# Performance work log

Measured on AMD Instinct MI355X. Metric: run time of the kernel, lower is better.

## Reference

```python
import jax, jax.numpy as jnp
import numpy as np

N = 100000      # nodes
E = 1600000     # edges
D = 128         # embedding_size (num_heads=1)
L = 4           # num_layers
NEG_SLOPE_ATT = 0.2    # GATConv attention LeakyReLU
NEG_SLOPE_ACT = 0.01   # nn.LeakyReLU default
LN_EPS = 1e-5


def leaky(x, s):
    return jnp.where(x > 0, x, s * x)


def layer_norm(x, gamma, beta):
    mu = jnp.mean(x, axis=-1, keepdims=True)
    var = jnp.mean(jnp.square(x - mu), axis=-1, keepdims=True)
    return (x - mu) * jax.lax.rsqrt(var + LN_EPS) * gamma + beta


def gat_conv(x, src, dst, W, a_src, a_dst, b):
    # PyG GATConv, heads=1, add_self_loops=False, no edge features
    h = x @ W                                  # [N, D]
    alpha_src = h @ a_src                      # [N]
    alpha_dst = h @ a_dst                      # [N]
    e = leaky(alpha_src[src] + alpha_dst[dst], NEG_SLOPE_ATT)   # [E]
    # softmax over incoming edges of each destination node
    m = jax.ops.segment_max(e, dst, num_segments=N)             # [N]
    ex = jnp.exp(e - m[dst])
    denom = jax.ops.segment_sum(ex, dst, num_segments=N)        # [N]
    alpha = ex / (denom[dst] + 1e-16)                           # [E]
    out = jax.ops.segment_sum(alpha[:, None] * h[src], dst, num_segments=N)
    return out + b


def setup_inputs() -> dict:
    key = jax.random.key(0)
    ks = jax.random.split(key, 12)
    x = jax.random.normal(ks[0], (N, D), dtype=jnp.float32)
    edge_index = jax.random.randint(ks[1], (2, E), 0, N, dtype=jnp.int32)
    s = 0.05
    return {
        "x": x,
        "edge_index": edge_index,
        "W_in": jax.random.normal(ks[2], (D, D), dtype=jnp.float32) * s,
        "b_in": jnp.zeros((D,), dtype=jnp.float32),
        "Wl": jax.random.normal(ks[3], (L, D, D), dtype=jnp.float32) * s,
        "att_src": jax.random.normal(ks[4], (L, D), dtype=jnp.float32) * s,
        "att_dst": jax.random.normal(ks[5], (L, D), dtype=jnp.float32) * s,
        "bias_l": jnp.zeros((L, D), dtype=jnp.float32),
        "gamma": jnp.ones((L, D), dtype=jnp.float32),
        "beta": jnp.zeros((L, D), dtype=jnp.float32),
    }


def reference(x, edge_index, W_in, b_in, Wl, att_src, att_dst, bias_l, gamma, beta):
    src, dst = edge_index[0], edge_index[1]
    h = leaky(x @ W_in + b_in, NEG_SLOPE_ACT)
    for i in range(L):
        h = gat_conv(h, src, dst, Wl[i], att_src[i], att_dst[i], bias_l[i])
        h = layer_norm(h, gamma[i], beta[i])
        h = leaky(h, NEG_SLOPE_ACT)
        # dropout p=0.3 is identity in eval mode; pooling undefined in source -> identity
    return h
```

## Files before the change

### kernel.cpp

```cpp
#include <hip/hip_runtime.h>
#include <hip/hip_fp16.h>
#include <math.h>

#define NN 100000
#define EE 1600000
#define DD 128
#define NBUCK 196
#define NBLKP 196
#define EPB 8192

typedef _Float16 f16;
typedef f16 f16x8 __attribute__((ext_vector_type(8)));
typedef float f32x4 __attribute__((ext_vector_type(4)));

#define LDA 136
#define WCHUNKS 2304

__global__ __launch_bounds__(256) void part_hist_k(const int* __restrict__ dst, int* __restrict__ bcnt) {
    __shared__ int lc[NBUCK];
    int t = threadIdx.x, blk = blockIdx.x;
    if (t < NBUCK) lc[t] = 0;
    __syncthreads();
    int e0 = blk * EPB;
    for (int i = t; i < EPB; i += 256) {
        int e = e0 + i;
        if (e < EE) atomicAdd(&lc[dst[e] >> 9], 1);
    }
    __syncthreads();
    if (t < NBUCK) bcnt[t * NBLKP + blk] = lc[t];
}

__global__ __launch_bounds__(256) void scanBB_k(const int* __restrict__ bcnt, int* __restrict__ ebase,
                                                int* __restrict__ btot) {
    __shared__ int sh[256];
    int t = threadIdx.x, b = blockIdx.x;
    int c = (t < NBLKP) ? bcnt[b * NBLKP + t] : 0;
    sh[t] = c;
    __syncthreads();
    for (int off = 1; off < 256; off <<= 1) {
        int v = (t >= off) ? sh[t - off] : 0;
        __syncthreads();
        sh[t] += v;
        __syncthreads();
    }
    if (t < NBLKP) ebase[b * NBLKP + t] = sh[t] - c;
    if (t == 255) btot[b] = sh[255];
}

__global__ __launch_bounds__(256) void scanBT_k(const int* __restrict__ btot, int* __restrict__ bstart,
                                                int* __restrict__ offsets) {
    __shared__ int sh[256];
    int t = threadIdx.x;
    int c = (t < NBUCK) ? btot[t] : 0;
    sh[t] = c;
    __syncthreads();
    for (int off = 1; off < 256; off <<= 1) {
        int v = (t >= off) ? sh[t - off] : 0;
        __syncthreads();
        sh[t] += v;
        __syncthreads();
    }
    if (t < NBUCK) bstart[t] = sh[t] - c;
    if (t == 0) { bstart[NBUCK] = EE; offsets[NN] = EE; }
}

__global__ __launch_bounds__(256) void part_k(const int* __restrict__ src, const int* __restrict__ dst,
                                              const int* __restrict__ bstart, const int* __restrict__ ebase,
                                              int2* __restrict__ ebuf) {
    __shared__ int cur[NBUCK];
    int t = threadIdx.x, blk = blockIdx.x;
    if (t < NBUCK) cur[t] = bstart[t] + ebase[t * NBLKP + blk];
    __syncthreads();
    int e0 = blk * EPB;
    for (int i = t; i < EPB; i += 256) {
        int e = e0 + i;
        if (e < EE) {
            int s = src[e], d = dst[e];
            int p = atomicAdd(&cur[d >> 9], 1);
            ebuf[p] = make_int2(s, d);
        }
    }
}

__global__ __launch_bounds__(512) void bucket_sort_k(const int2* __restrict__ ebuf,
                                                     const int* __restrict__ bstart,
                                                     int* __restrict__ offsets,
                                                     int* __restrict__ ssrc,
                                                     int* __restrict__ sdst) {
    __shared__ int sh[512];
    __shared__ int cur[512];
    int t = threadIdx.x, b = blockIdx.x;
    int d0 = b << 9;
    int beg = bstart[b], end = bstart[b + 1];

    cur[t] = 0;
    __syncthreads();
    for (int e = beg + t; e < end; e += 512) atomicAdd(&cur[ebuf[e].y - d0], 1);
    __syncthreads();
    int c = cur[t];
    sh[t] = c;
    __syncthreads();
    for (int off = 1; off < 512; off <<= 1) {
        int v = (t >= off) ? sh[t - off] : 0;
        __syncthreads();
        sh[t] += v;
        __syncthreads();
    }
    int excl = sh[t] - c;
    if (d0 + t < NN) offsets[d0 + t] = beg + excl;
    cur[t] = beg + excl;
    __syncthreads();
    for (int e = beg + t; e < end; e += 512) {
        int2 ed = ebuf[e];
        int p = atomicAdd(&cur[ed.y - d0], 1);
        ssrc[p] = ed.x;
        sdst[p] = ed.y;
    }
}

__global__ __launch_bounds__(256) void wprep_k(const float* __restrict__ W_in,
                                               const float* __restrict__ Wl,
                                               f16* __restrict__ Wt) {
    int m = blockIdx.x;
    const float* src = (m == 0) ? W_in : (Wl + (size_t)(m - 1) * DD * DD);
    f16* dst = Wt + (size_t)m * (WCHUNKS * 8);
    for (int q = 0; q < 64; ++q) {
        int idx = q * 256 + threadIdx.x;
        int k = idx >> 7, n = idx & 127;
        dst[n * LDA + k] = (f16)src[idx];
    }
}

template <int MODE, int F32IN>
__global__ __launch_bounds__(256, 2) void gemm_k(const void* __restrict__ Xv,
                                                 const f16* __restrict__ Wt,
                                                 const float* __restrict__ bias,
                                                 const float* __restrict__ av_src,
                                                 const float* __restrict__ av_dst,
                                                 __half* __restrict__ Yh,
                                                 float* __restrict__ alpha_src,
                                                 float* __restrict__ alpha_dst) {
    __shared__ __align__(16) f16 sA[128 * LDA];
    __shared__ __align__(16) f16 sW[WCHUNKS * 8];
    int t = threadIdx.x;
    int w = t >> 6, lane = t & 63;
    int row0 = blockIdx.x * 128;

    {
        const uint4* wsrc = (const uint4*)Wt;
        uint4* wdst = (uint4*)sW;
#pragma unroll
        for (int it = 0; it < 9; ++it) wdst[it * 256 + t] = wsrc[it * 256 + t];
    }
    if (F32IN) {
        const float* X = (const float*)Xv;
#pragma unroll
        for (int q = 0; q < 8; ++q) {
            int id = q * 256 + t;
            int r = id >> 4, c = id & 15;
            int grow = row0 + r;
            float4 a = make_float4(0.f, 0.f, 0.f, 0.f), b = a;
            if (grow < NN) {
                const float4* p = (const float4*)(X + (size_t)grow * DD + c * 8);
                a = p[0]; b = p[1];
            }
            union { f16 h[8]; uint4 u; } H;
            H.h[0] = (f16)a.x; H.h[1] = (f16)a.y; H.h[2] = (f16)a.z; H.h[3] = (f16)a.w;
            H.h[4] = (f16)b.x; H.h[5] = (f16)b.y; H.h[6] = (f16)b.z; H.h[7] = (f16)b.w;
            *(uint4*)(sA + r * LDA + c * 8) = H.u;
        }
    } else {
        const __half* X = (const __half*)Xv;
#pragma unroll
        for (int q = 0; q < 8; ++q) {
            int id = q * 256 + t;
            int r = id >> 4, c = id & 15;
            int grow = row0 + r;
            uint4 v = make_uint4(0, 0, 0, 0);
            if (grow < NN) v = ((const uint4*)(X + (size_t)grow * DD))[c];
            *(uint4*)(sA + r * LDA + c * 8) = v;
        }
    }
    __syncthreads();

    int cl = lane & 15, qw = lane >> 4;
    f32x4 acc[2][8] = {};
#pragma unroll
    for (int ks = 0; ks < 4; ++ks) {
        int koff = ks * 32 + qw * 8;
        f16x8 bh[8];
#pragma unroll
        for (int nf = 0; nf < 8; ++nf)
            bh[nf] = *(const f16x8*)(sW + (nf * 16 + cl) * LDA + koff);
#pragma unroll
        for (int rf = 0; rf < 2; ++rf) {
            f16x8 ah = *(const f16x8*)(sA + (w * 32 + rf * 16 + cl) * LDA + koff);
#pragma unroll
            for (int nf = 0; nf < 8; ++nf)
                acc[rf][nf] = __builtin_amdgcn_mfma_f32_16x16x32_f16(ah, bh[nf], acc[rf][nf], 0, 0, 0);
        }
    }

    if (MODE == 0) {
        float bc[8];
#pragma unroll
        for (int nf = 0; nf < 8; ++nf) bc[nf] = bias[nf * 16 + cl];
#pragma unroll
        for (int rf = 0; rf < 2; ++rf) {
            int rbase = row0 + w * 32 + rf * 16 + qw * 4;
#pragma unroll
            for (int i = 0; i < 4; ++i) {
                int row = rbase + i;
                if (row < NN) {
#pragma unroll
                    for (int nf = 0; nf < 8; ++nf) {
                        float v = acc[rf][nf][i] + bc[nf];
                        v = v > 0.f ? v : 0.01f * v;
                        Yh[(size_t)row * DD + nf * 16 + cl] = __float2half(v);
                    }
                }
            }
        }
    } else {
        float as[8], ad[8];
#pragma unroll
        for (int nf = 0; nf < 8; ++nf) {
            as[nf] = av_src[nf * 16 + cl];
            ad[nf] = av_dst[nf * 16 + cl];
        }
#pragma unroll
        for (int rf = 0; rf < 2; ++rf) {
            int rbase = row0 + w * 32 + rf * 16 + qw * 4;
            float pa[4] = {0.f, 0.f, 0.f, 0.f}, pb[4] = {0.f, 0.f, 0.f, 0.f};
#pragma unroll
            for (int nf = 0; nf < 8; ++nf) {
#pragma unroll
                for (int i = 0; i < 4; ++i) {
                    float v = acc[rf][nf][i];
                    pa[i] += v * as[nf];
                    pb[i] += v * ad[nf];
                }
            }
#pragma unroll
            for (int i = 0; i < 4; ++i) {
                int row = rbase + i;
                if (row < NN) {
#pragma unroll
                    for (int nf = 0; nf < 8; ++nf)
                        Yh[(size_t)row * DD + nf * 16 + cl] = __float2half(acc[rf][nf][i]);
                }
            }
#pragma unroll
            for (int i = 0; i < 4; ++i) {
#pragma unroll
                for (int off = 8; off >= 1; off >>= 1) {
                    pa[i] += __shfl_xor(pa[i], off);
                    pb[i] += __shfl_xor(pb[i], off);
                }
            }
            if (cl == 0) {
#pragma unroll
                for (int i = 0; i < 4; ++i) {
                    int row = rbase + i;
                    if (row < NN) {
                        alpha_src[row] = pa[i];
                        alpha_dst[row] = pb[i];
                    }
                }
            }
        }
    }
}

__global__ __launch_bounds__(256) void edgew_k(const int* __restrict__ ssrc,
                                               const int* __restrict__ sdst,
                                               const float* __restrict__ alpha_src,
                                               const float* __restrict__ alpha_dst,
                                               int2* __restrict__ epk) {
    int j = blockIdx.x * 256 + threadIdx.x;
    if (j < EE) {
        int s = ssrc[j];
        float e = alpha_src[s] + alpha_dst[sdst[j]];
        e = e > 0.f ? e : 0.2f * e;
        epk[j] = make_int2(s, __float_as_int(__expf(e)));
    } else if (j < EE + 16) {
        epk[j] = make_int2(0, 0);
    }
}

template <int HOUT>
__global__ __launch_bounds__(256) void agg_k(const __half* __restrict__ tmp,
                                             const int2* __restrict__ epk,
                                             const int* __restrict__ offsets,
                                             const float* __restrict__ bias,
                                             const float* __restrict__ gamma,
                                             const float* __restrict__ beta,
                                             void* __restrict__ outv) {
    int wid = (blockIdx.x * 256 + threadIdx.x) >> 6;
    wid = __builtin_amdgcn_readfirstlane(wid);
    int lane = threadIdx.x & 63;
    int beg = __builtin_amdgcn_readfirstlane(offsets[wid]);
    int end = __builtin_amdgcn_readfirstlane(offsets[wid + 1]);

    const __half2* tmp2 = (const __half2*)tmp;
    float ax0 = 0.f, ay0 = 0.f, ax1 = 0.f, ay1 = 0.f, dsum = 0.f;

    for (int j = (beg & ~1); j < end; j += 16) {
        int4 q[8];
#pragma unroll
        for (int k = 0; k < 8; ++k) q[k] = *(const int4*)(epk + j + 2 * k);
        __half2 h[16];
#pragma unroll
        for (int k = 0; k < 8; ++k) {
            h[2 * k]     = tmp2[(size_t)q[k].x * 64 + lane];
            h[2 * k + 1] = tmp2[(size_t)q[k].z * 64 + lane];
        }
#pragma unroll
        for (int k = 0; k < 8; ++k) {
            int e0 = j + 2 * k, e1 = e0 + 1;
            bool v0 = (k == 0) ? (e0 >= beg && e0 < end) : (e0 < end);
            bool v1 = (e1 < end);
            float w0 = v0 ? __int_as_float(q[k].y) : 0.f;
            float w1 = v1 ? __int_as_float(q[k].w) : 0.f;
            dsum += w0 + w1;
            ax0 = fmaf(w0, __half2float(h[2 * k].x), ax0);
            ay0 = fmaf(w0, __half2float(h[2 * k].y), ay0);
            ax1 = fmaf(w1, __half2float(h[2 * k + 1].x), ax1);
            ay1 = fmaf(w1, __half2float(h[2 * k + 1].y), ay1);
        }
    }

    float inv = 1.0f / (dsum + 1e-16f);

    float ax = (ax0 + ax1) * inv + bias[2 * lane];
    float ay = (ay0 + ay1) * inv + bias[2 * lane + 1];

    float s1 = ax + ay;
#pragma unroll
    for (int off = 32; off >= 1; off >>= 1) s1 += __shfl_xor(s1, off);
    float mu = s1 * (1.0f / 128.0f);
    float dx = ax - mu, dy = ay - mu;
    float s2 = dx * dx + dy * dy;
#pragma unroll
    for (int off = 32; off >= 1; off >>= 1) s2 += __shfl_xor(s2, off);
    float rstd = rsqrtf(s2 * (1.0f / 128.0f) + 1e-5f);

    float yx = dx * rstd * gamma[2 * lane] + beta[2 * lane];
    float yy = dy * rstd * gamma[2 * lane + 1] + beta[2 * lane + 1];
    yx = yx > 0.f ? yx : 0.01f * yx;
    yy = yy > 0.f ? yy : 0.01f * yy;
    if (HOUT) {
        ((__half2*)outv)[(size_t)wid * 64 + lane] = __floats2half2_rn(yx, yy);
    } else {
        ((float2*)outv)[(size_t)wid * 64 + lane] = make_float2(yx, yy);
    }
}

extern "C" void kernel_launch(void* const* d_in, const int* in_sizes, int n_in,
                              void* d_out, int out_size, void* d_ws, size_t ws_size,
                              hipStream_t stream) {
    const float* x       = (const float*)d_in[0];
    const int*   ei      = (const int*)d_in[1];
    const float* W_in    = (const float*)d_in[2];
    const float* b_in    = (const float*)d_in[3];
    const float* Wl      = (const float*)d_in[4];
    const float* att_src = (const float*)d_in[5];
    const float* att_dst = (const float*)d_in[6];
    const float* bias_l  = (const float*)d_in[7];
    const float* gamma   = (const float*)d_in[8];
    const float* beta    = (const float*)d_in[9];
    float* out = (float*)d_out;

    char* ws = (char*)d_ws;
    __half* tmp      = (__half*)ws; ws += (size_t)NN * DD * 2;
    float* alpha_src = (float*)ws;  ws += (size_t)NN * 4;
    float* alpha_dst = (float*)ws;  ws += (size_t)NN * 4;
    int*   offsets   = (int*)ws;    ws += (size_t)(NN + 4) * 4;
    int*   ssrc      = (int*)ws;    ws += (size_t)EE * 4;
    int*   sdst      = (int*)ws;    ws += (size_t)EE * 4;
    int2*  ebuf      = (int2*)ws;   ws += (size_t)(EE + 16) * 8;
    int*   bcnt      = (int*)ws;    ws += (size_t)NBUCK * NBLKP * 4;
    int*   ebase     = (int*)ws;    ws += (size_t)NBUCK * NBLKP * 4;
    int*   btot      = (int*)ws;    ws += (size_t)(NBUCK + 4) * 4;
    int*   bstart    = (int*)ws;    ws += (size_t)(NBUCK + 4) * 4;
    f16*   Wt        = (f16*)ws;    ws += (size_t)5 * WCHUNKS * 16;
    int2* epk = ebuf;

    __half* hbuf = (__half*)d_out;

    const int* esrc = ei;
    const int* edst = ei + EE;

    part_hist_k<<<NBLKP, 256, 0, stream>>>(edst, bcnt);
    scanBB_k<<<NBUCK, 256, 0, stream>>>(bcnt, ebase, btot);
    scanBT_k<<<1, 256, 0, stream>>>(btot, bstart, offsets);
    part_k<<<NBLKP, 256, 0, stream>>>(esrc, edst, bstart, ebase, ebuf);
    bucket_sort_k<<<NBUCK, 512, 0, stream>>>(ebuf, bstart, offsets, ssrc, sdst);
    wprep_k<<<5, 256, 0, stream>>>(W_in, Wl, Wt);

    const int gg = (NN + 127) / 128;
    const int eg = (EE + 16 + 255) / 256;

    gemm_k<0, 1><<<gg, 256, 0, stream>>>(x, Wt, b_in, nullptr, nullptr, hbuf, nullptr, nullptr);

    for (int i = 0; i < 4; i++) {
        gemm_k<1, 0><<<gg, 256, 0, stream>>>(hbuf, Wt + (size_t)(i + 1) * (WCHUNKS * 8), nullptr,
                                             att_src + (size_t)i * DD, att_dst + (size_t)i * DD,
                                             tmp, alpha_src, alpha_dst);
        edgew_k<<<eg, 256, 0, stream>>>(ssrc, sdst, alpha_src, alpha_dst, epk);
        if (i < 3) {
            agg_k<1><<<NN / 4, 256, 0, stream>>>(tmp, epk, offsets,
                                                 bias_l + (size_t)i * DD, gamma + (size_t)i * DD,
                                                 beta + (size_t)i * DD, (void*)hbuf);
        } else {
            agg_k<0><<<NN / 4, 256, 0, stream>>>(tmp, epk, offsets,
                                                 bias_l + (size_t)i * DD, gamma + (size_t)i * DD,
                                                 beta + (size_t)i * DD, (void*)out);
        }
    }
}
```

Before: 580.4 us.

## Load GEMM A operands directly to registers and split aggregation lanes across edge pairs

The GEMM kernel no longer stages the activation tile in shared memory. Each wave loads its A fragments straight from global memory into registers, and the occupancy hint rises to 3 blocks per CU. The aggregation kernel now has each half-wave handle alternate edges with 8-byte gathers of 4 features per lane. Each 16-edge chunk is accumulated with packed half-precision FMAs, then the two halves are combined with a cross-half shuffle. This cuts LDS traffic and the number of gather instructions, at the cost of reduced accumulation precision from fp16 partial sums.

```diff
diff --git a/kernel.cpp b/kernel.cpp
--- a/kernel.cpp
+++ b/kernel.cpp
@@ -132,7 +132,7 @@
 }
 
 template <int MODE, int F32IN>
-__global__ __launch_bounds__(256, 2) void gemm_k(const void* __restrict__ Xv,
+__global__ __launch_bounds__(256, 3) void gemm_k(const void* __restrict__ Xv,
                                                  const f16* __restrict__ Wt,
                                                  const float* __restrict__ bias,
                                                  const float* __restrict__ av_src,
@@ -140,11 +140,42 @@
                                                  __half* __restrict__ Yh,
                                                  float* __restrict__ alpha_src,
                                                  float* __restrict__ alpha_dst) {
-    __shared__ __align__(16) f16 sA[128 * LDA];
     __shared__ __align__(16) f16 sW[WCHUNKS * 8];
     int t = threadIdx.x;
     int w = t >> 6, lane = t & 63;
+    int cl = lane & 15, qw = lane >> 4;
     int row0 = blockIdx.x * 128;
+
+    f16x8 a[2][4];
+    if (F32IN) {
+        const float* X = (const float*)Xv;
+#pragma unroll
+        for (int rf = 0; rf < 2; ++rf) {
+            int row = row0 + w * 32 + rf * 16 + cl;
+            row = row < NN ? row : NN - 1;
+            const float* p = X + (size_t)row * DD;
+#pragma unroll
+            for (int ks = 0; ks < 4; ++ks) {
+                float4 u0 = *(const float4*)(p + ks * 32 + qw * 8);
+                float4 u1 = *(const float4*)(p + ks * 32 + qw * 8 + 4);
+                f16x8 v;
+                v[0] = (f16)u0.x; v[1] = (f16)u0.y; v[2] = (f16)u0.z; v[3] = (f16)u0.w;
+                v[4] = (f16)u1.x; v[5] = (f16)u1.y; v[6] = (f16)u1.z; v[7] = (f16)u1.w;
+                a[rf][ks] = v;
+            }
+        }
+    } else {
+        const f16* X = (const f16*)Xv;
+#pragma unroll
+        for (int rf = 0; rf < 2; ++rf) {
+            int row = row0 + w * 32 + rf * 16 + cl;
+            row = row < NN ? row : NN - 1;
+            const f16* p = X + (size_t)row * DD;
+#pragma unroll
+            for (int ks = 0; ks < 4; ++ks)
+                a[rf][ks] = *(const f16x8*)(p + ks * 32 + qw * 8);
+        }
+    }
 
     {
         const uint4* wsrc = (const uint4*)Wt;
@@ -152,52 +183,17 @@
 #pragma unroll
         for (int it = 0; it < 9; ++it) wdst[it * 256 + t] = wsrc[it * 256 + t];
     }
-    if (F32IN) {
-        const float* X = (const float*)Xv;
-#pragma unroll
-        for (int q = 0; q < 8; ++q) {
-            int id = q * 256 + t;
-            int r = id >> 4, c = id & 15;
-            int grow = row0 + r;
-            float4 a = make_float4(0.f, 0.f, 0.f, 0.f), b = a;
-            if (grow < NN) {
-                const float4* p = (const float4*)(X + (size_t)grow * DD + c * 8);
-                a = p[0]; b = p[1];
-            }
-            union { f16 h[8]; uint4 u; } H;
-            H.h[0] = (f16)a.x; H.h[1] = (f16)a.y; H.h[2] = (f16)a.z; H.h[3] = (f16)a.w;
-            H.h[4] = (f16)b.x; H.h[5] = (f16)b.y; H.h[6] = (f16)b.z; H.h[7] = (f16)b.w;
-            *(uint4*)(sA + r * LDA + c * 8) = H.u;
-        }
-    } else {
-        const __half* X = (const __half*)Xv;
-#pragma unroll
-        for (int q = 0; q < 8; ++q) {
-            int id = q * 256 + t;
-            int r = id >> 4, c = id & 15;
-            int grow = row0 + r;
-            uint4 v = make_uint4(0, 0, 0, 0);
-            if (grow < NN) v = ((const uint4*)(X + (size_t)grow * DD))[c];
-            *(uint4*)(sA + r * LDA + c * 8) = v;
-        }
-    }
-    __syncthreads();
-
-    int cl = lane & 15, qw = lane >> 4;
+    __syncthreads();
+
     f32x4 acc[2][8] = {};
 #pragma unroll
     for (int ks = 0; ks < 4; ++ks) {
         int koff = ks * 32 + qw * 8;
-        f16x8 bh[8];
-#pragma unroll
-        for (int nf = 0; nf < 8; ++nf)
-            bh[nf] = *(const f16x8*)(sW + (nf * 16 + cl) * LDA + koff);
-#pragma unroll
-        for (int rf = 0; rf < 2; ++rf) {
-            f16x8 ah = *(const f16x8*)(sA + (w * 32 + rf * 16 + cl) * LDA + koff);
-#pragma unroll
-            for (int nf = 0; nf < 8; ++nf)
-                acc[rf][nf] = __builtin_amdgcn_mfma_f32_16x16x32_f16(ah, bh[nf], acc[rf][nf], 0, 0, 0);
+#pragma unroll
+        for (int nf = 0; nf < 8; ++nf) {
+            f16x8 bh = *(const f16x8*)(sW + (nf * 16 + cl) * LDA + koff);
+            acc[0][nf] = __builtin_amdgcn_mfma_f32_16x16x32_f16(a[0][ks], bh, acc[0][nf], 0, 0, 0);
+            acc[1][nf] = __builtin_amdgcn_mfma_f32_16x16x32_f16(a[1][ks], bh, acc[1][nf], 0, 0, 0);
         }
     }
 
@@ -299,60 +295,84 @@
     int wid = (blockIdx.x * 256 + threadIdx.x) >> 6;
     wid = __builtin_amdgcn_readfirstlane(wid);
     int lane = threadIdx.x & 63;
+    int eh = lane >> 5;
+    int c  = lane & 31;
     int beg = __builtin_amdgcn_readfirstlane(offsets[wid]);
     int end = __builtin_amdgcn_readfirstlane(offsets[wid + 1]);
 
-    const __half2* tmp2 = (const __half2*)tmp;
-    float ax0 = 0.f, ay0 = 0.f, ax1 = 0.f, ay1 = 0.f, dsum = 0.f;
+    const char* tmpB = (const char*)tmp;
+    float fx0 = 0.f, fx1 = 0.f, fx2 = 0.f, fx3 = 0.f;
+    float dsum = 0.f;
 
     for (int j = (beg & ~1); j < end; j += 16) {
         int4 q[8];
 #pragma unroll
         for (int k = 0; k < 8; ++k) q[k] = *(const int4*)(epk + j + 2 * k);
-        __half2 h[16];
+        __half2 acc01 = __float2half2_rn(0.f);
+        __half2 acc23 = __float2half2_rn(0.f);
 #pragma unroll
         for (int k = 0; k < 8; ++k) {
-            h[2 * k]     = tmp2[(size_t)q[k].x * 64 + lane];
-            h[2 * k + 1] = tmp2[(size_t)q[k].z * 64 + lane];
-        }
-#pragma unroll
-        for (int k = 0; k < 8; ++k) {
-            int e0 = j + 2 * k, e1 = e0 + 1;
-            bool v0 = (k == 0) ? (e0 >= beg && e0 < end) : (e0 < end);
-            bool v1 = (e1 < end);
-            float w0 = v0 ? __int_as_float(q[k].y) : 0.f;
-            float w1 = v1 ? __int_as_float(q[k].w) : 0.f;
-            dsum += w0 + w1;
-            ax0 = fmaf(w0, __half2float(h[2 * k].x), ax0);
-            ay0 = fmaf(w0, __half2float(h[2 * k].y), ay0);
-            ax1 = fmaf(w1, __half2float(h[2 * k + 1].x), ax1);
-            ay1 = fmaf(w1, __half2float(h[2 * k + 1].y), ay1);
-        }
-    }
-
+            int e0 = j + 2 * k;
+            float we = ((k == 0 ? e0 >= beg : true) && e0 < end) ? __int_as_float(q[k].y) : 0.f;
+            float wo = (e0 + 1 < end) ? __int_as_float(q[k].w) : 0.f;
+            int   row = eh ? q[k].z : q[k].x;
+            float wv  = eh ? wo : we;
+            const __half2* p = (const __half2*)(tmpB + ((size_t)(unsigned)row << 8) + (c << 3));
+            __half2 h0 = p[0];
+            __half2 h1 = p[1];
+            dsum += wv;
+            __half2 wh2 = __half2half2(__float2half(wv));
+            acc01 = __hfma2(wh2, h0, acc01);
+            acc23 = __hfma2(wh2, h1, acc23);
+        }
+        float2 f01 = __half22float2(acc01);
+        float2 f23 = __half22float2(acc23);
+        fx0 += f01.x; fx1 += f01.y; fx2 += f23.x; fx3 += f23.y;
+    }
+
+    fx0 += __shfl_xor(fx0, 32);
+    fx1 += __shfl_xor(fx1, 32);
+    fx2 += __shfl_xor(fx2, 32);
+    fx3 += __shfl_xor(fx3, 32);
+    dsum += __shfl_xor(dsum, 32);
     float inv = 1.0f / (dsum + 1e-16f);
 
-    float ax = (ax0 + ax1) * inv + bias[2 * lane];
-    float ay = (ay0 + ay1) * inv + bias[2 * lane + 1];
-
-    float s1 = ax + ay;
-#pragma unroll
-    for (int off = 32; off >= 1; off >>= 1) s1 += __shfl_xor(s1, off);
+    float4 bi = *(const float4*)(bias + 4 * c);
+    float a0 = fx0 * inv + bi.x;
+    float a1 = fx1 * inv + bi.y;
+    float a2 = fx2 * inv + bi.z;
+    float a3 = fx3 * inv + bi.w;
+
+    float s1 = (a0 + a1) + (a2 + a3);
+#pragma unroll
+    for (int off = 16; off >= 1; off >>= 1) s1 += __shfl_xor(s1, off);
     float mu = s1 * (1.0f / 128.0f);
-    float dx = ax - mu, dy = ay - mu;
-    float s2 = dx * dx + dy * dy;
-#pragma unroll
-    for (int off = 32; off >= 1; off >>= 1) s2 += __shfl_xor(s2, off);
+    float d0 = a0 - mu, d1 = a1 - mu, d2 = a2 - mu, d3 = a3 - mu;
+    float s2 = (d0 * d0 + d1 * d1) + (d2 * d2 + d3 * d3);
+#pragma unroll
+    for (int off = 16; off >= 1; off >>= 1) s2 += __shfl_xor(s2, off);
     float rstd = rsqrtf(s2 * (1.0f / 128.0f) + 1e-5f);
 
-    float yx = dx * rstd * gamma[2 * lane] + beta[2 * lane];
-    float yy = dy * rstd * gamma[2 * lane + 1] + beta[2 * lane + 1];
-    yx = yx > 0.f ? yx : 0.01f * yx;
-    yy = yy > 0.f ? yy : 0.01f * yy;
-    if (HOUT) {
-        ((__half2*)outv)[(size_t)wid * 64 + lane] = __floats2half2_rn(yx, yy);
-    } else {
-        ((float2*)outv)[(size_t)wid * 64 + lane] = make_float2(yx, yy);
+    float4 g  = *(const float4*)(gamma + 4 * c);
+    float4 be = *(const float4*)(beta + 4 * c);
+    float y0 = d0 * rstd * g.x + be.x;
+    float y1 = d1 * rstd * g.y + be.y;
+    float y2 = d2 * rstd * g.z + be.z;
+    float y3 = d3 * rstd * g.w + be.w;
+    y0 = y0 > 0.f ? y0 : 0.01f * y0;
+    y1 = y1 > 0.f ? y1 : 0.01f * y1;
+    y2 = y2 > 0.f ? y2 : 0.01f * y2;
+    y3 = y3 > 0.f ? y3 : 0.01f * y3;
+
+    if (lane < 32) {
+        if (HOUT) {
+            union { __half2 h2[2]; uint2 u; } pk;
+            pk.h2[0] = __floats2half2_rn(y0, y1);
+            pk.h2[1] = __floats2half2_rn(y2, y3);
+            ((uint2*)outv)[(size_t)wid * 32 + c] = pk.u;
+        } else {
+            ((float4*)outv)[(size_t)wid * 32 + c] = make_float4(y0, y1, y2, y3);
+        }
     }
 }
 
```

New measurement: 576.7 us. Within noise of the previous version (-0.6%).

## Fuse input GEMM with first GAT GEMM and precompute W·att vectors

Applied to the files above, without the earlier changes.

Folds the input projection into the first layer GEMM, so the intermediate activation no longer takes a global round trip and one launch disappears. The attention logits are now taken as the input rows dotted with precomputed W·a vectors (built in wprep_k), not reduced from the fp32 accumulators. A-operand fragments are loaded straight from global into registers instead of being staged in LDS, and the output is staged through LDS for coalesced 16-byte stores. The logits now come from fp16-rounded inputs, which slightly changes numerics, and the per-block LDS footprint changes.

```diff
diff --git a/kernel.cpp b/kernel.cpp
--- a/kernel.cpp
+++ b/kernel.cpp
@@ -120,7 +120,10 @@
 
 __global__ __launch_bounds__(256) void wprep_k(const float* __restrict__ W_in,
                                                const float* __restrict__ Wl,
-                                               f16* __restrict__ Wt) {
+                                               const float* __restrict__ att_src,
+                                               const float* __restrict__ att_dst,
+                                               f16* __restrict__ Wt,
+                                               float* __restrict__ wav) {
     int m = blockIdx.x;
     const float* src = (m == 0) ? W_in : (Wl + (size_t)(m - 1) * DD * DD);
     f16* dst = Wt + (size_t)m * (WCHUNKS * 8);
@@ -129,146 +132,171 @@
         int k = idx >> 7, n = idx & 127;
         dst[n * LDA + k] = (f16)src[idx];
     }
-}
-
-template <int MODE, int F32IN>
+    if (m >= 1) {
+        int t = threadIdx.x;
+        const float* av = (t < 128) ? (att_src + (size_t)(m - 1) * DD)
+                                    : (att_dst + (size_t)(m - 1) * DD);
+        int k = t & 127;
+        float s = 0.f;
+        for (int n = 0; n < 128; ++n) s += src[k * 128 + n] * av[n];
+        wav[(size_t)(m - 1) * 256 + (t >> 7) * 128 + k] = s;
+    }
+}
+
+template <int FUSED>
 __global__ __launch_bounds__(256, 2) void gemm_k(const void* __restrict__ Xv,
-                                                 const f16* __restrict__ Wt,
+                                                 const f16* __restrict__ Wt0,
+                                                 const f16* __restrict__ Wt1,
                                                  const float* __restrict__ bias,
-                                                 const float* __restrict__ av_src,
-                                                 const float* __restrict__ av_dst,
+                                                 const float* __restrict__ wa_s,
+                                                 const float* __restrict__ wa_d,
                                                  __half* __restrict__ Yh,
                                                  float* __restrict__ alpha_src,
                                                  float* __restrict__ alpha_dst) {
-    __shared__ __align__(16) f16 sA[128 * LDA];
     __shared__ __align__(16) f16 sW[WCHUNKS * 8];
+    __shared__ __align__(16) f16 sOut[4][32][LDA];
     int t = threadIdx.x;
     int w = t >> 6, lane = t & 63;
+    int cl = lane & 15, qw = lane >> 4;
     int row0 = blockIdx.x * 128;
 
+    f16x8 a[2][4];
+    if (FUSED) {
+        const float* X = (const float*)Xv;
+#pragma unroll
+        for (int rf = 0; rf < 2; ++rf) {
+            int row = row0 + w * 32 + rf * 16 + cl;
+            row = row < NN ? row : NN - 1;
+            const float* p = X + (size_t)row * DD;
+#pragma unroll
+            for (int ks = 0; ks < 4; ++ks) {
+                float4 u0 = *(const float4*)(p + ks * 32 + qw * 8);
+                float4 u1 = *(const float4*)(p + ks * 32 + qw * 8 + 4);
+                f16x8 v;
+                v[0] = (f16)u0.x; v[1] = (f16)u0.y; v[2] = (f16)u0.z; v[3] = (f16)u0.w;
+                v[4] = (f16)u1.x; v[5] = (f16)u1.y; v[6] = (f16)u1.z; v[7] = (f16)u1.w;
+                a[rf][ks] = v;
+            }
+        }
+    } else {
+        const f16* X = (const f16*)Xv;
+#pragma unroll
+        for (int rf = 0; rf < 2; ++rf) {
+            int row = row0 + w * 32 + rf * 16 + cl;
+            row = row < NN ? row : NN - 1;
+            const f16* p = X + (size_t)row * DD;
+#pragma unroll
+            for (int ks = 0; ks < 4; ++ks)
+                a[rf][ks] = *(const f16x8*)(p + ks * 32 + qw * 8);
+        }
+    }
+
     {
-        const uint4* wsrc = (const uint4*)Wt;
+        const uint4* wsrc = (const uint4*)Wt0;
         uint4* wdst = (uint4*)sW;
 #pragma unroll
         for (int it = 0; it < 9; ++it) wdst[it * 256 + t] = wsrc[it * 256 + t];
     }
-    if (F32IN) {
-        const float* X = (const float*)Xv;
-#pragma unroll
-        for (int q = 0; q < 8; ++q) {
-            int id = q * 256 + t;
-            int r = id >> 4, c = id & 15;
-            int grow = row0 + r;
-            float4 a = make_float4(0.f, 0.f, 0.f, 0.f), b = a;
-            if (grow < NN) {
-                const float4* p = (const float4*)(X + (size_t)grow * DD + c * 8);
-                a = p[0]; b = p[1];
-            }
-            union { f16 h[8]; uint4 u; } H;
-            H.h[0] = (f16)a.x; H.h[1] = (f16)a.y; H.h[2] = (f16)a.z; H.h[3] = (f16)a.w;
-            H.h[4] = (f16)b.x; H.h[5] = (f16)b.y; H.h[6] = (f16)b.z; H.h[7] = (f16)b.w;
-            *(uint4*)(sA + r * LDA + c * 8) = H.u;
-        }
-    } else {
-        const __half* X = (const __half*)Xv;
-#pragma unroll
-        for (int q = 0; q < 8; ++q) {
-            int id = q * 256 + t;
-            int r = id >> 4, c = id & 15;
-            int grow = row0 + r;
-            uint4 v = make_uint4(0, 0, 0, 0);
-            if (grow < NN) v = ((const uint4*)(X + (size_t)grow * DD))[c];
-            *(uint4*)(sA + r * LDA + c * 8) = v;
-        }
-    }
-    __syncthreads();
-
-    int cl = lane & 15, qw = lane >> 4;
+    __syncthreads();
+
     f32x4 acc[2][8] = {};
 #pragma unroll
     for (int ks = 0; ks < 4; ++ks) {
         int koff = ks * 32 + qw * 8;
-        f16x8 bh[8];
-#pragma unroll
-        for (int nf = 0; nf < 8; ++nf)
-            bh[nf] = *(const f16x8*)(sW + (nf * 16 + cl) * LDA + koff);
-#pragma unroll
-        for (int rf = 0; rf < 2; ++rf) {
-            f16x8 ah = *(const f16x8*)(sA + (w * 32 + rf * 16 + cl) * LDA + koff);
+#pragma unroll
+        for (int nf = 0; nf < 8; ++nf) {
+            f16x8 bh = *(const f16x8*)(sW + (nf * 16 + cl) * LDA + koff);
+            acc[0][nf] = __builtin_amdgcn_mfma_f32_16x16x32_f16(a[0][ks], bh, acc[0][nf], 0, 0, 0);
+            acc[1][nf] = __builtin_amdgcn_mfma_f32_16x16x32_f16(a[1][ks], bh, acc[1][nf], 0, 0, 0);
+        }
+    }
+
+    if (FUSED) {
+        __syncthreads();
+        {
+            const uint4* wsrc = (const uint4*)Wt1;
+            uint4* wdst = (uint4*)sW;
+#pragma unroll
+            for (int it = 0; it < 9; ++it) wdst[it * 256 + t] = wsrc[it * 256 + t];
+        }
+        float bc[8];
+#pragma unroll
+        for (int nf = 0; nf < 8; ++nf) bc[nf] = bias[nf * 16 + cl];
+#pragma unroll
+        for (int rf = 0; rf < 2; ++rf)
+#pragma unroll
+            for (int i = 0; i < 4; ++i)
+#pragma unroll
+                for (int nf = 0; nf < 8; ++nf) {
+                    float v = acc[rf][nf][i] + bc[nf];
+                    v = v > 0.f ? v : 0.01f * v;
+                    sOut[w][rf * 16 + qw * 4 + i][nf * 16 + cl] = (f16)v;
+                }
+        __syncthreads();
+#pragma unroll
+        for (int rf = 0; rf < 2; ++rf)
+#pragma unroll
+            for (int ks = 0; ks < 4; ++ks)
+                a[rf][ks] = *(const f16x8*)&sOut[w][rf * 16 + cl][ks * 32 + qw * 8];
+#pragma unroll
+        for (int rf = 0; rf < 2; ++rf)
 #pragma unroll
             for (int nf = 0; nf < 8; ++nf)
-                acc[rf][nf] = __builtin_amdgcn_mfma_f32_16x16x32_f16(ah, bh[nf], acc[rf][nf], 0, 0, 0);
-        }
-    }
-
-    if (MODE == 0) {
-        float bc[8];
-#pragma unroll
-        for (int nf = 0; nf < 8; ++nf) bc[nf] = bias[nf * 16 + cl];
-#pragma unroll
-        for (int rf = 0; rf < 2; ++rf) {
-            int rbase = row0 + w * 32 + rf * 16 + qw * 4;
-#pragma unroll
-            for (int i = 0; i < 4; ++i) {
-                int row = rbase + i;
-                if (row < NN) {
-#pragma unroll
-                    for (int nf = 0; nf < 8; ++nf) {
-                        float v = acc[rf][nf][i] + bc[nf];
-                        v = v > 0.f ? v : 0.01f * v;
-                        Yh[(size_t)row * DD + nf * 16 + cl] = __float2half(v);
-                    }
-                }
+                acc[rf][nf] = (f32x4){0.f, 0.f, 0.f, 0.f};
+#pragma unroll
+        for (int ks = 0; ks < 4; ++ks) {
+            int koff = ks * 32 + qw * 8;
+#pragma unroll
+            for (int nf = 0; nf < 8; ++nf) {
+                f16x8 bh = *(const f16x8*)(sW + (nf * 16 + cl) * LDA + koff);
+                acc[0][nf] = __builtin_amdgcn_mfma_f32_16x16x32_f16(a[0][ks], bh, acc[0][nf], 0, 0, 0);
+                acc[1][nf] = __builtin_amdgcn_mfma_f32_16x16x32_f16(a[1][ks], bh, acc[1][nf], 0, 0, 0);
             }
         }
-    } else {
-        float as[8], ad[8];
-#pragma unroll
-        for (int nf = 0; nf < 8; ++nf) {
-            as[nf] = av_src[nf * 16 + cl];
-            ad[nf] = av_dst[nf * 16 + cl];
-        }
-#pragma unroll
-        for (int rf = 0; rf < 2; ++rf) {
-            int rbase = row0 + w * 32 + rf * 16 + qw * 4;
-            float pa[4] = {0.f, 0.f, 0.f, 0.f}, pb[4] = {0.f, 0.f, 0.f, 0.f};
-#pragma unroll
-            for (int nf = 0; nf < 8; ++nf) {
-#pragma unroll
-                for (int i = 0; i < 4; ++i) {
-                    float v = acc[rf][nf][i];
-                    pa[i] += v * as[nf];
-                    pb[i] += v * ad[nf];
-                }
+    }
+
+#pragma unroll
+    for (int rf = 0; rf < 2; ++rf) {
+        float pa = 0.f, pb = 0.f;
+#pragma unroll
+        for (int ks = 0; ks < 4; ++ks) {
+            const float* ps = wa_s + ks * 32 + qw * 8;
+            const float* pd = wa_d + ks * 32 + qw * 8;
+            float4 s0 = *(const float4*)ps, s1 = *(const float4*)(ps + 4);
+            float4 d0 = *(const float4*)pd, d1 = *(const float4*)(pd + 4);
+            float sv[8] = {s0.x, s0.y, s0.z, s0.w, s1.x, s1.y, s1.z, s1.w};
+            float dv[8] = {d0.x, d0.y, d0.z, d0.w, d1.x, d1.y, d1.z, d1.w};
+#pragma unroll
+            for (int e = 0; e < 8; ++e) {
+                float f = (float)a[rf][ks][e];
+                pa = fmaf(f, sv[e], pa);
+                pb = fmaf(f, dv[e], pb);
             }
-#pragma unroll
-            for (int i = 0; i < 4; ++i) {
-                int row = rbase + i;
-                if (row < NN) {
-#pragma unroll
-                    for (int nf = 0; nf < 8; ++nf)
-                        Yh[(size_t)row * DD + nf * 16 + cl] = __float2half(acc[rf][nf][i]);
-                }
+        }
+        pa += __shfl_xor(pa, 16); pa += __shfl_xor(pa, 32);
+        pb += __shfl_xor(pb, 16); pb += __shfl_xor(pb, 32);
+        if (qw == 0) {
+            int row = row0 + w * 32 + rf * 16 + cl;
+            if (row < NN) {
+                alpha_src[row] = pa;
+                alpha_dst[row] = pb;
             }
-#pragma unroll
-            for (int i = 0; i < 4; ++i) {
-#pragma unroll
-                for (int off = 8; off >= 1; off >>= 1) {
-                    pa[i] += __shfl_xor(pa[i], off);
-                    pb[i] += __shfl_xor(pb[i], off);
-                }
-            }
-            if (cl == 0) {
-#pragma unroll
-                for (int i = 0; i < 4; ++i) {
-                    int row = rbase + i;
-                    if (row < NN) {
-                        alpha_src[row] = pa[i];
-                        alpha_dst[row] = pb[i];
-                    }
-                }
-            }
-        }
+        }
+    }
+
+#pragma unroll
+    for (int rf = 0; rf < 2; ++rf)
+#pragma unroll
+        for (int i = 0; i < 4; ++i)
+#pragma unroll
+            for (int nf = 0; nf < 8; ++nf)
+                sOut[w][rf * 16 + qw * 4 + i][nf * 16 + cl] = (f16)acc[rf][nf][i];
+#pragma unroll
+    for (int p = 0; p < 8; ++p) {
+        int rl = p * 4 + qw;
+        uint4 v = *(const uint4*)&sOut[w][rl][cl * 8];
+        int row = row0 + w * 32 + rl;
+        if (row < NN) *(uint4*)(Yh + (size_t)row * DD + cl * 8) = v;
     }
 }
 
@@ -384,6 +412,7 @@
     int*   btot      = (int*)ws;    ws += (size_t)(NBUCK + 4) * 4;
     int*   bstart    = (int*)ws;    ws += (size_t)(NBUCK + 4) * 4;
     f16*   Wt        = (f16*)ws;    ws += (size_t)5 * WCHUNKS * 16;
+    float* wav       = (float*)ws;  ws += (size_t)4 * 256 * 4;
     int2* epk = ebuf;
 
     __half* hbuf = (__half*)d_out;
@@ -396,17 +425,20 @@
     scanBT_k<<<1, 256, 0, stream>>>(btot, bstart, offsets);
     part_k<<<NBLKP, 256, 0, stream>>>(esrc, edst, bstart, ebase, ebuf);
     bucket_sort_k<<<NBUCK, 512, 0, stream>>>(ebuf, bstart, offsets, ssrc, sdst);
-    wprep_k<<<5, 256, 0, stream>>>(W_in, Wl, Wt);
+    wprep_k<<<5, 256, 0, stream>>>(W_in, Wl, att_src, att_dst, Wt, wav);
 
     const int gg = (NN + 127) / 128;
     const int eg = (EE + 16 + 255) / 256;
 
-    gemm_k<0, 1><<<gg, 256, 0, stream>>>(x, Wt, b_in, nullptr, nullptr, hbuf, nullptr, nullptr);
-
-    for (int i = 0; i < 4; i++) {
-        gemm_k<1, 0><<<gg, 256, 0, stream>>>(hbuf, Wt + (size_t)(i + 1) * (WCHUNKS * 8), nullptr,
-                                             att_src + (size_t)i * DD, att_dst + (size_t)i * DD,
-                                             tmp, alpha_src, alpha_dst);
+    gemm_k<1><<<gg, 256, 0, stream>>>(x, Wt, Wt + (size_t)1 * (WCHUNKS * 8), b_in,
+                                      wav, wav + 128, tmp, alpha_src, alpha_dst);
+    edgew_k<<<eg, 256, 0, stream>>>(ssrc, sdst, alpha_src, alpha_dst, epk);
+    agg_k<1><<<NN / 4, 256, 0, stream>>>(tmp, epk, offsets, bias_l, gamma, beta, (void*)hbuf);
+
+    for (int i = 1; i < 4; i++) {
+        gemm_k<0><<<gg, 256, 0, stream>>>(hbuf, Wt + (size_t)(i + 1) * (WCHUNKS * 8), nullptr, nullptr,
+                                          wav + (size_t)i * 256, wav + (size_t)i * 256 + 128,
+                                          tmp, alpha_src, alpha_dst);
         edgew_k<<<eg, 256, 0, stream>>>(ssrc, sdst, alpha_src, alpha_dst, epk);
         if (i < 3) {
             agg_k<1><<<NN / 4, 256, 0, stream>>>(tmp, epk, offsets,
```

New measurement: 547.2 us. 5.7% less time.
